# Kernel optimization log

Measured on AMD Instinct MI355X. Metric: run time of the kernel, lower is better.

Reference implementation:

```python
import jax, jax.numpy as jnp
import numpy as np

B, C, H, W = 2, 256, 64, 64
NUM_HEADS = 8


def setup_inputs() -> dict:
    key = jax.random.key(0)
    k1, k2, k3 = jax.random.split(key, 3)
    x = jax.random.normal(k1, (B, C, H, W), dtype=jnp.float32)
    # 1x1 convs, bias=False -> plain [out_ch, in_ch] matrices
    w_qkv = jax.random.normal(k2, (3 * C, C), dtype=jnp.float32) * (1.0 / np.sqrt(C))
    w_proj = jax.random.normal(k3, (C, C), dtype=jnp.float32) * (1.0 / np.sqrt(C))
    return {"x": x, "w_qkv": w_qkv, "w_proj": w_proj}


def reference(x, w_qkv, w_proj):
    b, c, h, w = x.shape
    hd = NUM_HEADS
    d = c // hd  # head dim
    n = h * w    # number of tokens

    # 1x1 conv == channel matmul: [3C, C] x [B, C, H, W] -> [B, 3C, H, W]
    qkv = jnp.einsum('oc,bchw->bohw', w_qkv, x)
    q, k, v = jnp.split(qkv, 3, axis=1)

    def reshape(t):
        return t.reshape(b, hd, d, n)  # [B, h, d, N]

    q, k, v = map(reshape, (q, k, v))

    # scores[b,h,i,j] = sum_d q[b,h,d,i] * k[b,h,d,j] / sqrt(d)
    scores = jnp.einsum('bhdi,bhdj->bhij', q, k) / jnp.sqrt(jnp.asarray(d, x.dtype))
    attn = jax.nn.softmax(scores, axis=-1)

    # out[b,h,d,i] = sum_j attn[b,h,i,j] * v[b,h,d,j]
    out = jnp.einsum('bhij,bhdj->bhdi', attn, v)
    out = out.reshape(b, c, h, w)

    return jnp.einsum('oc,bchw->bohw', w_proj, out) + x
```

## Files before the change

### kernel.cpp

```cpp
#include <hip/hip_runtime.h>
#include <hip/hip_bf16.h>

#define NB  2
#define CC  256
#define NHD 8
#define HD  32
#define NT  4096

typedef __bf16 bf16x8 __attribute__((ext_vector_type(8)));
typedef bf16x8 bf16x8_ma __attribute__((may_alias));
typedef __bf16 bf16x4 __attribute__((ext_vector_type(4)));
typedef bf16x4 bf16x4_ma __attribute__((may_alias));
typedef float  f32x4  __attribute__((ext_vector_type(4)));
typedef f32x4  f32x4_ma __attribute__((may_alias));
typedef float  f32x16 __attribute__((ext_vector_type(16)));
typedef unsigned int u32x4 __attribute__((ext_vector_type(4)));
typedef unsigned short u16x8 __attribute__((ext_vector_type(8)));

static __device__ __forceinline__ f32x4 zero4() {
    f32x4 z = {0.f, 0.f, 0.f, 0.f}; return z;
}
static __device__ __forceinline__ f32x16 zero16() {
    f32x16 z = {0.f,0.f,0.f,0.f,0.f,0.f,0.f,0.f,
                0.f,0.f,0.f,0.f,0.f,0.f,0.f,0.f};
    return z;
}

#define QSCALE 0.25505392421795654f

#define CVT_PK(dst, lo, hi_) \
    asm("v_cvt_pk_bf16_f32 %0, %1, %2" : "=v"(dst) : "v"(lo), "v"(hi_))
#define PLSWAP(x, y) \
    asm("v_permlane32_swap_b32 %0, %1" : "+v"(x), "+v"(y))


__global__ __launch_bounds__(256) void convw_k(const float* __restrict__ s1,
                                               __bf16* __restrict__ d1, int n1,
                                               const float* __restrict__ s2,
                                               __bf16* __restrict__ d2, int n2) {
    const int i = blockIdx.x * 256 + threadIdx.x;
    if (i < n1) d1[i] = (__bf16)s1[i];
    else if (i - n1 < n2) d2[i - n1] = (__bf16)s2[i - n1];
}

__global__ __launch_bounds__(256) void transpose_k(const float* __restrict__ x,
                                                   __bf16* __restrict__ xt) {
    __shared__ __bf16 T[64][65];
    const int tid = threadIdx.x;
    const int n0 = blockIdx.x * 64, c0 = blockIdx.y * 64, b = blockIdx.z;

#pragma unroll
    for (int rep = 0; rep < 16; ++rep) {
        const int e = rep * 256 + tid;
        const int cl = e >> 6, nl = e & 63;
        T[nl][cl] = (__bf16)x[((size_t)(b * CC + c0 + cl)) * NT + n0 + nl];
    }
    __syncthreads();
#pragma unroll
    for (int rep = 0; rep < 16; ++rep) {
        const int e = rep * 256 + tid;
        const int nl = e >> 6, cl = e & 63;
        xt[((size_t)(b * NT + n0 + nl)) * CC + c0 + cl] = T[nl][cl];
    }
}

__global__ __launch_bounds__(256) void qkv_k(const __bf16* __restrict__ wqkv,
                                             const __bf16* __restrict__ xt,
                                             __bf16* __restrict__ qt,
                                             __bf16* __restrict__ kt,
                                             __bf16* __restrict__ vv) {
    __shared__ __align__(16) __bf16 BF[4][8][512];

    const int lane = threadIdx.x & 63, wv = threadIdx.x >> 6;
    const int g = lane >> 4, c16 = lane & 15;
    const int b    = blockIdx.z;
    const int o0   = blockIdx.y * 64 + wv * 16;
    const int tok0 = blockIdx.x * 64;

    const __bf16* bsrc = xt + ((size_t)(b * NT + tok0 + wv * 16 + c16)) * CC + g * 8;
#pragma unroll
    for (int kc = 0; kc < 8; ++kc) {
        __builtin_amdgcn_global_load_lds(
            (const __attribute__((address_space(1))) void*)(bsrc + kc * 32),
            (__attribute__((address_space(3))) void*)&BF[wv][kc][0],
            16, 0, 0);
    }

    const __bf16* arow = wqkv + (size_t)(o0 + c16) * CC + g * 8;
    bf16x8 a[8];
#pragma unroll
    for (int kc = 0; kc < 8; ++kc) a[kc] = *(const bf16x8_ma*)(arow + kc * 32);

    __syncthreads();

    f32x4 acc[4];
#pragma unroll
    for (int i = 0; i < 4; ++i) acc[i] = zero4();

#pragma unroll
    for (int kc = 0; kc < 8; ++kc) {
#pragma unroll
        for (int js = 0; js < 4; ++js) {
            bf16x8 bb = *(const bf16x8_ma*)&BF[js][kc][lane * 8];
            acc[js] = __builtin_amdgcn_mfma_f32_16x16x32_bf16(a[kc], bb, acc[js], 0, 0, 0);
        }
    }

    const int reg = o0 >> 8;
    const int oo0 = (o0 & 255) + g * 4;
    const int h   = oo0 >> 5;
    const int dd0 = oo0 & 31;
    const size_t bh = (size_t)(b * NHD + h);

#pragma unroll
    for (int js = 0; js < 4; ++js) {
        const int tok = tok0 + js * 16 + c16;
        if (reg == 0) {
            bf16x4 pk;
#pragma unroll
            for (int r = 0; r < 4; ++r) pk[r] = (__bf16)(acc[js][r] * QSCALE);
            *(bf16x4_ma*)(qt + (bh * NT + tok) * HD + dd0) = pk;
        } else if (reg == 1) {
            bf16x4 pk;
#pragma unroll
            for (int r = 0; r < 4; ++r) pk[r] = (__bf16)acc[js][r];
            *(bf16x4_ma*)(kt + (bh * NT + tok) * HD + dd0) = pk;
        } else {
#pragma unroll
            for (int r = 0; r < 4; ++r)
                vv[(bh * HD + dd0 + r) * NT + tok] = (__bf16)acc[js][r];
        }
    }
}

__global__ __launch_bounds__(256, 4) void attn_k(const __bf16* __restrict__ qt,
                                                 const __bf16* __restrict__ kt,
                                                 const __bf16* __restrict__ vv,
                                                 __bf16* __restrict__ ao,
                                                 float* __restrict__ PO,
                                                 float* __restrict__ PL) {
    __shared__ __align__(16) __bf16 KF[2][2][2][512];
    __shared__ __align__(16) __bf16 VF[2][2][2][512];

    const int tid  = threadIdx.x;
    const int lane = tid & 63, wv = tid >> 6;
    const int c32 = lane & 31, hi = lane >> 5;
    const int bh = blockIdx.y;
    const int b = bh >> 3, h = bh & 7;
    const int seg = blockIdx.z, nseg = gridDim.z;
    const int i0q = blockIdx.x * 128 + wv * 32;

    const __bf16* qbase = qt + ((size_t)bh * NT + i0q) * HD;
    const __bf16* kbase = kt + (size_t)bh * NT * HD;
    const __bf16* vbase = vv + (size_t)bh * HD * NT;

    const int stg_js = wv & 1, stg_sl = wv >> 1;

    bf16x8 aq0 = *(const bf16x8_ma*)(qbase + (size_t)c32 * HD + hi * 8);
    bf16x8 aq1 = *(const bf16x8_ma*)(qbase + (size_t)c32 * HD + 16 + hi * 8);

    u16x8 ones_u = {0x3F80,0x3F80,0x3F80,0x3F80,0x3F80,0x3F80,0x3F80,0x3F80};
    const bf16x8 ones = __builtin_bit_cast(bf16x8, ones_u);

    f32x16 oacc = zero16();
    f32x16 lacc = zero16();

#define STAGE(bf, jb) do {                                                              \
    const __bf16* gk = kbase + (size_t)((jb) + stg_js * 32 + c32) * HD                  \
                             + stg_sl * 16 + hi * 8;                                    \
    __builtin_amdgcn_global_load_lds(                                                   \
        (const __attribute__((address_space(1))) void*)gk,                              \
        (__attribute__((address_space(3))) void*)&KF[bf][stg_js][stg_sl][0],            \
        16, 0, 0);                                                                      \
    const __bf16* gv = vbase + (size_t)c32 * NT + (jb) + stg_js * 32                    \
                             + stg_sl * 16 + hi * 8;                                    \
    __builtin_amdgcn_global_load_lds(                                                   \
        (const __attribute__((address_space(1))) void*)gv,                              \
        (__attribute__((address_space(3))) void*)&VF[bf][stg_js][stg_sl][0],            \
        16, 0, 0);                                                                      \
} while (0)

#define SUBTILE(bf, js) do {                                                            \
    bf16x8 fk0 = *(const bf16x8_ma*)&KF[bf][js][0][lane * 8];                           \
    bf16x8 fk1 = *(const bf16x8_ma*)&KF[bf][js][1][lane * 8];                           \
    bf16x8 fv0 = *(const bf16x8_ma*)&VF[bf][js][0][lane * 8];                           \
    bf16x8 fv1 = *(const bf16x8_ma*)&VF[bf][js][1][lane * 8];                           \
    f32x16 s = __builtin_amdgcn_mfma_f32_32x32x16_bf16(fk0, aq0, zero16(), 0, 0, 0);    \
    s = __builtin_amdgcn_mfma_f32_32x32x16_bf16(fk1, aq1, s, 0, 0, 0);                  \
    float p[16];                                                                        \
    _Pragma("unroll")                                                                   \
    for (int r = 0; r < 16; ++r) p[r] = __builtin_amdgcn_exp2f(s[r]);                   \
    unsigned pk[8];                                                                     \
    _Pragma("unroll")                                                                   \
    for (int i = 0; i < 8; ++i) CVT_PK(pk[i], p[2 * i], p[2 * i + 1]);                  \
    PLSWAP(pk[0], pk[2]);                                                               \
    PLSWAP(pk[1], pk[3]);                                                               \
    PLSWAP(pk[4], pk[6]);                                                               \
    PLSWAP(pk[5], pk[7]);                                                               \
    u32x4 a0 = {pk[0], pk[1], pk[2], pk[3]};                                            \
    u32x4 a1 = {pk[4], pk[5], pk[6], pk[7]};                                            \
    const bf16x8 ap0 = __builtin_bit_cast(bf16x8, a0);                                  \
    const bf16x8 ap1 = __builtin_bit_cast(bf16x8, a1);                                  \
    oacc = __builtin_amdgcn_mfma_f32_32x32x16_bf16(ap0, fv0, oacc, 0, 0, 0);            \
    oacc = __builtin_amdgcn_mfma_f32_32x32x16_bf16(ap1, fv1, oacc, 0, 0, 0);            \
    lacc = __builtin_amdgcn_mfma_f32_32x32x16_bf16(ap0, ones, lacc, 0, 0, 0);           \
    lacc = __builtin_amdgcn_mfma_f32_32x32x16_bf16(ap1, ones, lacc, 0, 0, 0);           \
} while (0)

    const int ntiles  = (NT / 64) / nseg;
    const int j_begin = seg * ntiles * 64;

    STAGE(0, j_begin);
    asm volatile("s_waitcnt vmcnt(0)" ::: "memory");
    __syncthreads();

    int buf = 0;
#pragma unroll 1
    for (int t = 0; t < ntiles; ++t) {
        if (t + 1 < ntiles) STAGE(buf ^ 1, j_begin + (t + 1) * 64);
        SUBTILE(buf, 0);
        SUBTILE(buf, 1);
        asm volatile("s_waitcnt vmcnt(0)" ::: "memory");
        __syncthreads();
        buf ^= 1;
    }

#undef STAGE
#undef SUBTILE

    if (nseg == 1) {
#pragma unroll
        for (int g4 = 0; g4 < 4; ++g4) {
#pragma unroll
            for (int r = 0; r < 4; ++r) {
                const int q = 8 * g4 + 4 * hi + r;
                ao[((size_t)(b * NT) + i0q + q) * CC + h * HD + c32] =
                    (__bf16)(oacc[4 * g4 + r] / lacc[4 * g4 + r]);
            }
        }
    } else {
        float* po = PO + (((size_t)seg * NB * NHD + bh) * NT + i0q) * HD;
#pragma unroll
        for (int g4 = 0; g4 < 4; ++g4) {
#pragma unroll
            for (int r = 0; r < 4; ++r) {
                const int q = 8 * g4 + 4 * hi + r;
                po[(size_t)q * HD + c32] = oacc[4 * g4 + r];
            }
        }
        if (c32 == 0) {
            float* pl = PL + ((size_t)seg * NB * NHD + bh) * NT + i0q;
#pragma unroll
            for (int g4 = 0; g4 < 4; ++g4)
#pragma unroll
                for (int r = 0; r < 4; ++r)
                    pl[8 * g4 + 4 * hi + r] = lacc[4 * g4 + r];
        }
    }
}

__global__ __launch_bounds__(256) void comb_k(const float* __restrict__ PO,
                                              const float* __restrict__ PL,
                                              __bf16* __restrict__ ao) {
    const int i = blockIdx.x * 256 + threadIdx.x;
    const int bh = i >> 15;
    const int rem = i & 32767;
    const int n = rem >> 3, g = rem & 7;
    const int b = bh >> 3, h = bh & 7;

    const size_t o0i = (((size_t)bh) * NT + n) * HD + g * 4;
    const size_t o1i = o0i + (size_t)(NB * NHD) * NT * HD;
    f32x4 o0 = *(const f32x4_ma*)&PO[o0i];
    f32x4 o1 = *(const f32x4_ma*)&PO[o1i];
    const float l = PL[(size_t)bh * NT + n] + PL[(size_t)(NB * NHD) * NT + (size_t)bh * NT + n];

    bf16x4 pk;
#pragma unroll
    for (int r = 0; r < 4; ++r) pk[r] = (__bf16)((o0[r] + o1[r]) / l);
    *(bf16x4_ma*)&ao[((size_t)(b * NT) + n) * CC + h * HD + g * 4] = pk;
}

__global__ __launch_bounds__(256) void proj_k(const __bf16* __restrict__ wp,
                                              const __bf16* __restrict__ ao,
                                              const float* __restrict__ x,
                                              float* __restrict__ out) {
    __shared__ __align__(16) __bf16 BF[4][8][512];

    const int lane = threadIdx.x & 63, wv = threadIdx.x >> 6;
    const int g = lane >> 4, c16 = lane & 15;
    const int b    = blockIdx.z;
    const int o0   = blockIdx.y * 64 + wv * 16;
    const int tok0 = blockIdx.x * 64;

    const __bf16* bsrc = ao + ((size_t)(b * NT + tok0 + wv * 16 + c16)) * CC + g * 8;
#pragma unroll
    for (int kc = 0; kc < 8; ++kc) {
        __builtin_amdgcn_global_load_lds(
            (const __attribute__((address_space(1))) void*)(bsrc + kc * 32),
            (__attribute__((address_space(3))) void*)&BF[wv][kc][0],
            16, 0, 0);
    }

    const __bf16* arow = wp + (size_t)(o0 + c16) * CC + g * 8;
    bf16x8 a[8];
#pragma unroll
    for (int kc = 0; kc < 8; ++kc) a[kc] = *(const bf16x8_ma*)(arow + kc * 32);

    __syncthreads();

    f32x4 acc[4];
#pragma unroll
    for (int i = 0; i < 4; ++i) acc[i] = zero4();

#pragma unroll
    for (int kc = 0; kc < 8; ++kc) {
#pragma unroll
        for (int js = 0; js < 4; ++js) {
            bf16x8 bb = *(const bf16x8_ma*)&BF[js][kc][lane * 8];
            acc[js] = __builtin_amdgcn_mfma_f32_16x16x32_bf16(a[kc], bb, acc[js], 0, 0, 0);
        }
    }

#pragma unroll
    for (int js = 0; js < 4; ++js) {
        const int tok = tok0 + js * 16 + c16;
#pragma unroll
        for (int r = 0; r < 4; ++r) {
            const int o = o0 + g * 4 + r;
            const size_t idx = ((size_t)(b * CC + o)) * NT + tok;
            out[idx] = acc[js][r] + x[idx];
        }
    }
}

extern "C" void kernel_launch(void* const* d_in, const int* in_sizes, int n_in,
                              void* d_out, int out_size, void* d_ws, size_t ws_size,
                              hipStream_t stream) {
    const int SX  = NB * CC * NT;
    const int SW3 = 3 * CC * CC;
    const int SW1 = CC * CC;
    const size_t E = (size_t)SX;

    const float* x  = nullptr;
    const float* wq = nullptr;
    const float* wp = nullptr;
    for (int i = 0; i < n_in; ++i) {
        const int sz = in_sizes[i];
        if (sz == SX || sz == 2 * SX || sz == 4 * SX)           x  = (const float*)d_in[i];
        else if (sz == SW3 || sz == 2 * SW3 || sz == 4 * SW3)   wq = (const float*)d_in[i];
        else if (sz == SW1 || sz == 2 * SW1 || sz == 4 * SW1)   wp = (const float*)d_in[i];
    }
    if (!x || !wq || !wp) {
        x  = (const float*)d_in[0];
        wq = (const float*)d_in[1];
        wp = (const float*)d_in[2];
    }

    __bf16* ws  = (__bf16*)d_ws;
    __bf16* wqb = ws;
    __bf16* wpb = wqb + SW3;
    __bf16* xt  = wpb + SW1;
    __bf16* qt  = xt + E;
    __bf16* kt  = qt + E;
    __bf16* vv  = kt + E;
    __bf16* ao  = xt;

    const size_t baseB = (size_t)(SW3 + SW1) * 2 + 4 * E * 2;
    const size_t poB   = 2ull * NB * NHD * NT * HD * 4;
    const size_t plB   = 2ull * NB * NHD * NT * 4;
    const int jseg = (ws_size >= baseB + poB + plB) ? 2 : 1;
    float* PO = (float*)((char*)d_ws + baseB);
    float* PL = (float*)((char*)d_ws + baseB + poB);

    float* out = (float*)d_out;

    convw_k<<<dim3((SW3 + SW1 + 255) / 256), 256, 0, stream>>>(wq, wqb, SW3, wp, wpb, SW1);
    transpose_k<<<dim3(NT / 64, CC / 64, NB), 256, 0, stream>>>(x, xt);
    qkv_k<<<dim3(NT / 64, (3 * CC) / 64, NB), 256, 0, stream>>>(wqb, xt, qt, kt, vv);
    attn_k<<<dim3(NT / 128, NB * NHD, jseg), 256, 0, stream>>>(qt, kt, vv, ao, PO, PL);
    if (jseg == 2)
        comb_k<<<dim3((NB * NHD * NT * (HD / 4)) / 256), 256, 0, stream>>>(PO, PL, ao);
    proj_k<<<dim3(NT / 64, CC / 64, NB), 256, 0, stream>>>(wpb, ao, x, out);
}
```

Baseline: 143.5 us.

## Fuse split-K combine into projection and double attention K/V tile size

The attention kernel now stages 128 keys per iteration (each wave loads its own 32-key slice) and runs four subtiles between barriers, halving the number of barrier/sync points. The separate combine kernel is removed: a new projection kernel reads the two partial outputs and row sums, normalizes, packs to bf16 into shared memory and then does the projection GEMM. This drops one launch and the bf16 attention-output round trip through global memory. In exchange, LDS use doubles, and each projection block now redundantly reads partial fp32 data for its 64 tokens across four output-channel blocks.

```diff
diff --git a/kernel.cpp b/kernel.cpp
--- a/kernel.cpp
+++ b/kernel.cpp
@@ -139,8 +139,8 @@
                                                  __bf16* __restrict__ ao,
                                                  float* __restrict__ PO,
                                                  float* __restrict__ PL) {
-    __shared__ __align__(16) __bf16 KF[2][2][2][512];
-    __shared__ __align__(16) __bf16 VF[2][2][2][512];
+    __shared__ __align__(16) __bf16 KF[2][4][2][512];
+    __shared__ __align__(16) __bf16 VF[2][4][2][512];
 
     const int tid  = threadIdx.x;
     const int lane = tid & 63, wv = tid >> 6;
@@ -154,8 +154,6 @@
     const __bf16* kbase = kt + (size_t)bh * NT * HD;
     const __bf16* vbase = vv + (size_t)bh * HD * NT;
 
-    const int stg_js = wv & 1, stg_sl = wv >> 1;
-
     bf16x8 aq0 = *(const bf16x8_ma*)(qbase + (size_t)c32 * HD + hi * 8);
     bf16x8 aq1 = *(const bf16x8_ma*)(qbase + (size_t)c32 * HD + 16 + hi * 8);
 
@@ -166,17 +164,23 @@
     f32x16 lacc = zero16();
 
 #define STAGE(bf, jb) do {                                                              \
-    const __bf16* gk = kbase + (size_t)((jb) + stg_js * 32 + c32) * HD                  \
-                             + stg_sl * 16 + hi * 8;                                    \
+    const __bf16* gk = kbase + (size_t)((jb) + wv * 32 + c32) * HD + hi * 8;            \
     __builtin_amdgcn_global_load_lds(                                                   \
         (const __attribute__((address_space(1))) void*)gk,                              \
-        (__attribute__((address_space(3))) void*)&KF[bf][stg_js][stg_sl][0],            \
+        (__attribute__((address_space(3))) void*)&KF[bf][wv][0][0],                     \
         16, 0, 0);                                                                      \
-    const __bf16* gv = vbase + (size_t)c32 * NT + (jb) + stg_js * 32                    \
-                             + stg_sl * 16 + hi * 8;                                    \
+    __builtin_amdgcn_global_load_lds(                                                   \
+        (const __attribute__((address_space(1))) void*)(gk + 16),                       \
+        (__attribute__((address_space(3))) void*)&KF[bf][wv][1][0],                     \
+        16, 0, 0);                                                                      \
+    const __bf16* gv = vbase + (size_t)c32 * NT + (jb) + wv * 32 + hi * 8;              \
     __builtin_amdgcn_global_load_lds(                                                   \
         (const __attribute__((address_space(1))) void*)gv,                              \
-        (__attribute__((address_space(3))) void*)&VF[bf][stg_js][stg_sl][0],            \
+        (__attribute__((address_space(3))) void*)&VF[bf][wv][0][0],                     \
+        16, 0, 0);                                                                      \
+    __builtin_amdgcn_global_load_lds(                                                   \
+        (const __attribute__((address_space(1))) void*)(gv + 16),                       \
+        (__attribute__((address_space(3))) void*)&VF[bf][wv][1][0],                     \
         16, 0, 0);                                                                      \
 } while (0)
 
@@ -207,8 +211,8 @@
     lacc = __builtin_amdgcn_mfma_f32_32x32x16_bf16(ap1, ones, lacc, 0, 0, 0);           \
 } while (0)
 
-    const int ntiles  = (NT / 64) / nseg;
-    const int j_begin = seg * ntiles * 64;
+    const int ntiles  = (NT / 128) / nseg;
+    const int j_begin = seg * ntiles * 128;
 
     STAGE(0, j_begin);
     asm volatile("s_waitcnt vmcnt(0)" ::: "memory");
@@ -217,9 +221,11 @@
     int buf = 0;
 #pragma unroll 1
     for (int t = 0; t < ntiles; ++t) {
-        if (t + 1 < ntiles) STAGE(buf ^ 1, j_begin + (t + 1) * 64);
+        if (t + 1 < ntiles) STAGE(buf ^ 1, j_begin + (t + 1) * 128);
         SUBTILE(buf, 0);
         SUBTILE(buf, 1);
+        SUBTILE(buf, 2);
+        SUBTILE(buf, 3);
         asm volatile("s_waitcnt vmcnt(0)" ::: "memory");
         __syncthreads();
         buf ^= 1;
@@ -259,27 +265,6 @@
     }
 }
 
-__global__ __launch_bounds__(256) void comb_k(const float* __restrict__ PO,
-                                              const float* __restrict__ PL,
-                                              __bf16* __restrict__ ao) {
-    const int i = blockIdx.x * 256 + threadIdx.x;
-    const int bh = i >> 15;
-    const int rem = i & 32767;
-    const int n = rem >> 3, g = rem & 7;
-    const int b = bh >> 3, h = bh & 7;
-
-    const size_t o0i = (((size_t)bh) * NT + n) * HD + g * 4;
-    const size_t o1i = o0i + (size_t)(NB * NHD) * NT * HD;
-    f32x4 o0 = *(const f32x4_ma*)&PO[o0i];
-    f32x4 o1 = *(const f32x4_ma*)&PO[o1i];
-    const float l = PL[(size_t)bh * NT + n] + PL[(size_t)(NB * NHD) * NT + (size_t)bh * NT + n];
-
-    bf16x4 pk;
-#pragma unroll
-    for (int r = 0; r < 4; ++r) pk[r] = (__bf16)((o0[r] + o1[r]) / l);
-    *(bf16x4_ma*)&ao[((size_t)(b * NT) + n) * CC + h * HD + g * 4] = pk;
-}
-
 __global__ __launch_bounds__(256) void proj_k(const __bf16* __restrict__ wp,
                                               const __bf16* __restrict__ ao,
                                               const float* __restrict__ x,
@@ -305,6 +290,73 @@
     bf16x8 a[8];
 #pragma unroll
     for (int kc = 0; kc < 8; ++kc) a[kc] = *(const bf16x8_ma*)(arow + kc * 32);
+
+    __syncthreads();
+
+    f32x4 acc[4];
+#pragma unroll
+    for (int i = 0; i < 4; ++i) acc[i] = zero4();
+
+#pragma unroll
+    for (int kc = 0; kc < 8; ++kc) {
+#pragma unroll
+        for (int js = 0; js < 4; ++js) {
+            bf16x8 bb = *(const bf16x8_ma*)&BF[js][kc][lane * 8];
+            acc[js] = __builtin_amdgcn_mfma_f32_16x16x32_bf16(a[kc], bb, acc[js], 0, 0, 0);
+        }
+    }
+
+#pragma unroll
+    for (int js = 0; js < 4; ++js) {
+        const int tok = tok0 + js * 16 + c16;
+#pragma unroll
+        for (int r = 0; r < 4; ++r) {
+            const int o = o0 + g * 4 + r;
+            const size_t idx = ((size_t)(b * CC + o)) * NT + tok;
+            out[idx] = acc[js][r] + x[idx];
+        }
+    }
+}
+
+__global__ __launch_bounds__(256) void projc_k(const __bf16* __restrict__ wp,
+                                               const float* __restrict__ PO,
+                                               const float* __restrict__ PL,
+                                               const float* __restrict__ x,
+                                               float* __restrict__ out) {
+    __shared__ __align__(16) __bf16 BF[4][8][512];
+
+    const int lane = threadIdx.x & 63, wv = threadIdx.x >> 6;
+    const int g = lane >> 4, c16 = lane & 15;
+    const int b    = blockIdx.z;
+    const int o0   = blockIdx.y * 64 + wv * 16;
+    const int tok0 = blockIdx.x * 64;
+
+    const __bf16* arow = wp + (size_t)(o0 + c16) * CC + g * 8;
+    bf16x8 a[8];
+#pragma unroll
+    for (int kc = 0; kc < 8; ++kc) a[kc] = *(const bf16x8_ma*)(arow + kc * 32);
+
+    const int ntok = tok0 + wv * 16 + c16;
+    const size_t SEGO = (size_t)(NB * NHD) * NT * HD;
+    const size_t SEGL = (size_t)(NB * NHD) * NT;
+#pragma unroll
+    for (int kc = 0; kc < 8; ++kc) {
+        const size_t bhn = (size_t)(b * NHD + kc) * NT + ntok;
+        const size_t poi = bhn * HD + g * 8;
+        f32x4 oa0 = *(const f32x4_ma*)&PO[poi];
+        f32x4 ob0 = *(const f32x4_ma*)&PO[poi + 4];
+        f32x4 oa1 = *(const f32x4_ma*)&PO[SEGO + poi];
+        f32x4 ob1 = *(const f32x4_ma*)&PO[SEGO + poi + 4];
+        const float l = PL[bhn] + PL[SEGL + bhn];
+        const float rl = 1.0f / l;
+        unsigned pk[4];
+        CVT_PK(pk[0], (oa0[0] + oa1[0]) * rl, (oa0[1] + oa1[1]) * rl);
+        CVT_PK(pk[1], (oa0[2] + oa1[2]) * rl, (oa0[3] + oa1[3]) * rl);
+        CVT_PK(pk[2], (ob0[0] + ob1[0]) * rl, (ob0[1] + ob1[1]) * rl);
+        CVT_PK(pk[3], (ob0[2] + ob1[2]) * rl, (ob0[3] + ob1[3]) * rl);
+        u32x4 u = {pk[0], pk[1], pk[2], pk[3]};
+        *(bf16x8_ma*)&BF[wv][kc][lane * 8] = __builtin_bit_cast(bf16x8, u);
+    }
 
     __syncthreads();
 
@@ -379,6 +431,7 @@
     qkv_k<<<dim3(NT / 64, (3 * CC) / 64, NB), 256, 0, stream>>>(wqb, xt, qt, kt, vv);
     attn_k<<<dim3(NT / 128, NB * NHD, jseg), 256, 0, stream>>>(qt, kt, vv, ao, PO, PL);
     if (jseg == 2)
-        comb_k<<<dim3((NB * NHD * NT * (HD / 4)) / 256), 256, 0, stream>>>(PO, PL, ao);
-    proj_k<<<dim3(NT / 64, CC / 64, NB), 256, 0, stream>>>(wpb, ao, x, out);
-}
+        projc_k<<<dim3(NT / 64, CC / 64, NB), 256, 0, stream>>>(wpb, PO, PL, x, out);
+    else
+        proj_k<<<dim3(NT / 64, CC / 64, NB), 256, 0, stream>>>(wpb, ao, x, out);
+}
```

Result: no change. 144.7 us (+0.8%).

## Widen attention key tile to 128 and allow four-way key split

Applied to the files above, without the earlier changes.

The attention kernel now stages 128 keys per iteration instead of 64, with each wave loading a full 32-key slice, and runs four subtiles per barrier. The key range can be split into up to four segments when the workspace is large enough, and the combine kernel sums a variable number of partials. The aim is fewer barriers per key and more blocks in flight (512 instead of 256) so the GPU is better filled. In exchange, shared memory per block and the fp32 partial traffic handled by the combine kernel both grow.

```diff
diff --git a/kernel.cpp b/kernel.cpp
--- a/kernel.cpp
+++ b/kernel.cpp
@@ -139,8 +139,8 @@
                                                  __bf16* __restrict__ ao,
                                                  float* __restrict__ PO,
                                                  float* __restrict__ PL) {
-    __shared__ __align__(16) __bf16 KF[2][2][2][512];
-    __shared__ __align__(16) __bf16 VF[2][2][2][512];
+    __shared__ __align__(16) __bf16 KF[2][4][2][512];
+    __shared__ __align__(16) __bf16 VF[2][4][2][512];
 
     const int tid  = threadIdx.x;
     const int lane = tid & 63, wv = tid >> 6;
@@ -154,8 +154,6 @@
     const __bf16* kbase = kt + (size_t)bh * NT * HD;
     const __bf16* vbase = vv + (size_t)bh * HD * NT;
 
-    const int stg_js = wv & 1, stg_sl = wv >> 1;
-
     bf16x8 aq0 = *(const bf16x8_ma*)(qbase + (size_t)c32 * HD + hi * 8);
     bf16x8 aq1 = *(const bf16x8_ma*)(qbase + (size_t)c32 * HD + 16 + hi * 8);
 
@@ -166,17 +164,23 @@
     f32x16 lacc = zero16();
 
 #define STAGE(bf, jb) do {                                                              \
-    const __bf16* gk = kbase + (size_t)((jb) + stg_js * 32 + c32) * HD                  \
-                             + stg_sl * 16 + hi * 8;                                    \
+    const __bf16* gk = kbase + (size_t)((jb) + wv * 32 + c32) * HD + hi * 8;            \
     __builtin_amdgcn_global_load_lds(                                                   \
         (const __attribute__((address_space(1))) void*)gk,                              \
-        (__attribute__((address_space(3))) void*)&KF[bf][stg_js][stg_sl][0],            \
+        (__attribute__((address_space(3))) void*)&KF[bf][wv][0][0],                     \
         16, 0, 0);                                                                      \
-    const __bf16* gv = vbase + (size_t)c32 * NT + (jb) + stg_js * 32                    \
-                             + stg_sl * 16 + hi * 8;                                    \
+    __builtin_amdgcn_global_load_lds(                                                   \
+        (const __attribute__((address_space(1))) void*)(gk + 16),                       \
+        (__attribute__((address_space(3))) void*)&KF[bf][wv][1][0],                     \
+        16, 0, 0);                                                                      \
+    const __bf16* gv = vbase + (size_t)c32 * NT + (jb) + wv * 32 + hi * 8;              \
     __builtin_amdgcn_global_load_lds(                                                   \
         (const __attribute__((address_space(1))) void*)gv,                              \
-        (__attribute__((address_space(3))) void*)&VF[bf][stg_js][stg_sl][0],            \
+        (__attribute__((address_space(3))) void*)&VF[bf][wv][0][0],                     \
+        16, 0, 0);                                                                      \
+    __builtin_amdgcn_global_load_lds(                                                   \
+        (const __attribute__((address_space(1))) void*)(gv + 16),                       \
+        (__attribute__((address_space(3))) void*)&VF[bf][wv][1][0],                     \
         16, 0, 0);                                                                      \
 } while (0)
 
@@ -207,8 +211,8 @@
     lacc = __builtin_amdgcn_mfma_f32_32x32x16_bf16(ap1, ones, lacc, 0, 0, 0);           \
 } while (0)
 
-    const int ntiles  = (NT / 64) / nseg;
-    const int j_begin = seg * ntiles * 64;
+    const int ntiles  = (NT / 128) / nseg;
+    const int j_begin = seg * ntiles * 128;
 
     STAGE(0, j_begin);
     asm volatile("s_waitcnt vmcnt(0)" ::: "memory");
@@ -217,9 +221,11 @@
     int buf = 0;
 #pragma unroll 1
     for (int t = 0; t < ntiles; ++t) {
-        if (t + 1 < ntiles) STAGE(buf ^ 1, j_begin + (t + 1) * 64);
+        if (t + 1 < ntiles) STAGE(buf ^ 1, j_begin + (t + 1) * 128);
         SUBTILE(buf, 0);
         SUBTILE(buf, 1);
+        SUBTILE(buf, 2);
+        SUBTILE(buf, 3);
         asm volatile("s_waitcnt vmcnt(0)" ::: "memory");
         __syncthreads();
         buf ^= 1;
@@ -261,22 +267,30 @@
 
 __global__ __launch_bounds__(256) void comb_k(const float* __restrict__ PO,
                                               const float* __restrict__ PL,
-                                              __bf16* __restrict__ ao) {
+                                              __bf16* __restrict__ ao,
+                                              int nseg) {
     const int i = blockIdx.x * 256 + threadIdx.x;
     const int bh = i >> 15;
     const int rem = i & 32767;
     const int n = rem >> 3, g = rem & 7;
     const int b = bh >> 3, h = bh & 7;
 
+    const size_t SEGO = (size_t)(NB * NHD) * NT * HD;
+    const size_t SEGL = (size_t)(NB * NHD) * NT;
     const size_t o0i = (((size_t)bh) * NT + n) * HD + g * 4;
-    const size_t o1i = o0i + (size_t)(NB * NHD) * NT * HD;
-    f32x4 o0 = *(const f32x4_ma*)&PO[o0i];
-    f32x4 o1 = *(const f32x4_ma*)&PO[o1i];
-    const float l = PL[(size_t)bh * NT + n] + PL[(size_t)(NB * NHD) * NT + (size_t)bh * NT + n];
+    const size_t li  = (size_t)bh * NT + n;
+
+    f32x4 o = *(const f32x4_ma*)&PO[o0i];
+    float l = PL[li];
+#pragma unroll 3
+    for (int s = 1; s < nseg; ++s) {
+        o += *(const f32x4_ma*)&PO[(size_t)s * SEGO + o0i];
+        l += PL[(size_t)s * SEGL + li];
+    }
 
     bf16x4 pk;
 #pragma unroll
-    for (int r = 0; r < 4; ++r) pk[r] = (__bf16)((o0[r] + o1[r]) / l);
+    for (int r = 0; r < 4; ++r) pk[r] = (__bf16)(o[r] / l);
     *(bf16x4_ma*)&ao[((size_t)(b * NT) + n) * CC + h * HD + g * 4] = pk;
 }
 
@@ -366,11 +380,13 @@
     __bf16* ao  = xt;
 
     const size_t baseB = (size_t)(SW3 + SW1) * 2 + 4 * E * 2;
-    const size_t poB   = 2ull * NB * NHD * NT * HD * 4;
-    const size_t plB   = 2ull * NB * NHD * NT * 4;
-    const int jseg = (ws_size >= baseB + poB + plB) ? 2 : 1;
+    const size_t segoB = (size_t)NB * NHD * NT * HD * 4;
+    const size_t seglB = (size_t)NB * NHD * NT * 4;
+    int jseg = 1;
+    if (ws_size >= baseB + 4 * (segoB + seglB)) jseg = 4;
+    else if (ws_size >= baseB + 2 * (segoB + seglB)) jseg = 2;
     float* PO = (float*)((char*)d_ws + baseB);
-    float* PL = (float*)((char*)d_ws + baseB + poB);
+    float* PL = (float*)((char*)d_ws + baseB + (size_t)jseg * segoB);
 
     float* out = (float*)d_out;
 
@@ -378,7 +394,7 @@
     transpose_k<<<dim3(NT / 64, CC / 64, NB), 256, 0, stream>>>(x, xt);
     qkv_k<<<dim3(NT / 64, (3 * CC) / 64, NB), 256, 0, stream>>>(wqb, xt, qt, kt, vv);
     attn_k<<<dim3(NT / 128, NB * NHD, jseg), 256, 0, stream>>>(qt, kt, vv, ao, PO, PL);
-    if (jseg == 2)
-        comb_k<<<dim3((NB * NHD * NT * (HD / 4)) / 256), 256, 0, stream>>>(PO, PL, ao);
+    if (jseg > 1)
+        comb_k<<<dim3((NB * NHD * NT * (HD / 4)) / 256), 256, 0, stream>>>(PO, PL, ao, jseg);
     proj_k<<<dim3(NT / 64, CC / 64, NB), 256, 0, stream>>>(wpb, ao, x, out);
 }
```

Measured after the change: 144.6 us. No clear change (+0.7%).
